# Optimization experiments

Measured on AMD Instinct MI355X. Metric: run time of the kernel, lower is better.

The kernel has to match this reference:

```python
import jax, jax.numpy as jnp
import numpy as np

D_MODEL, N_HEADS, D_HEAD = 512, 8, 64
NUM_BITS, C_TABLES, PHI_SCALE, MAX_EXP, EPS = 8, 2, 0.1, 4, 1e-6
B, T = 2, 1024


def setup_inputs() -> dict:
    key = jax.random.key(0)
    ks = jax.random.split(key, 7)
    x = jax.random.normal(ks[0], (B, T, D_MODEL), dtype=jnp.float32)
    w_std = 0.02
    Wq = jax.random.normal(ks[1], (D_MODEL, D_MODEL), dtype=jnp.float32) * w_std
    Wk = jax.random.normal(ks[2], (D_MODEL, D_MODEL), dtype=jnp.float32) * w_std
    Wv = jax.random.normal(ks[3], (D_MODEL, D_MODEL), dtype=jnp.float32) * w_std
    Wo = jax.random.normal(ks[4], (D_MODEL, D_MODEL), dtype=jnp.float32) * w_std
    bo = jnp.zeros((D_MODEL,), dtype=jnp.float32)
    # 'positive' init: strictly positive lookup values so phi acts as a kernel feature map
    phi_table = jax.random.uniform(ks[5], (C_TABLES, 2 ** NUM_BITS), dtype=jnp.float32) * 0.5 + 0.01
    return {"x": x, "Wq": Wq, "Wk": Wk, "Wv": Wv, "Wo": Wo, "bo": bo, "phi_table": phi_table}


def _ternary_weight(W):
    # quantize to {-1,0,1} * power-of-two scale (exponent clipped to +/- MAX_EXP), STE-style
    alpha = jnp.mean(jnp.abs(W)) + 1e-12
    e = jnp.clip(jnp.round(jnp.log2(alpha)), -MAX_EXP, MAX_EXP)
    s = jnp.exp2(e)
    Wt = jnp.clip(jnp.round(W / s), -1.0, 1.0) * s
    return W + jax.lax.stop_gradient(Wt - W)


def _ternary_linear(x, W, b=None):
    y = jnp.einsum('btd,ed->bte', x, _ternary_weight(W))
    return y if b is None else y + b


def _phi(x, table):
    # structured lookup activation: sum of c sub-tables indexed at dyadically scaled quantizations
    L = table.shape[1]
    off = L // 2
    y = jnp.zeros_like(x)
    for j in range(table.shape[0]):
        idx = jnp.clip(jnp.round(x / (PHI_SCALE * (2.0 ** j))).astype(jnp.int32) + off, 0, L - 1)
        y = y + table[j][idx]
    return x + jax.lax.stop_gradient(y - x)  # STE: forward = lookup, backward = identity


def reference(x, Wq, Wk, Wv, Wo, bo, phi_table):
    Bsz, Tn, _ = x.shape
    Q = _ternary_linear(x, Wq)
    K = _ternary_linear(x, Wk)
    V = _ternary_linear(x, Wv)

    def split_heads(t):
        return t.reshape(Bsz, Tn, N_HEADS, D_HEAD).transpose(0, 2, 1, 3)  # (B,H,T,d)

    Q, K, V = split_heads(Q), split_heads(K), split_heads(V)
    phiQ = _phi(Q, phi_table)
    phiK = _phi(K, phi_table)

    # causal linear attention via cumulative outer products (faithful to original)
    kv = jnp.einsum('bhnd,bhne->bhnde', phiK, V)            # (B,H,T,d,d)
    kv_cum = jnp.cumsum(kv, axis=2)
    out = jnp.einsum('bhnd,bhnde->bhne', phiQ, kv_cum)       # (B,H,T,d)
    k_cum = jnp.cumsum(phiK, axis=2)
    Z = jnp.clip(jnp.sum(phiQ * k_cum, axis=-1, keepdims=True), EPS, None)
    out = out / Z

    out = out.transpose(0, 2, 1, 3).reshape(Bsz, Tn, D_MODEL)
    return _ternary_linear(out, Wo, bo)
```

## Files before the change

### kernel.cpp

```cpp
#include <hip/hip_runtime.h>
#include <stdint.h>

typedef __bf16 bf16;
typedef __bf16 v8bf __attribute__((ext_vector_type(8)));
typedef float v4f __attribute__((ext_vector_type(4)));

#define T_SEQ   1024
#define D_MODEL 512
#define N_HEADS 8
#define D_HEAD  64
#define B_SZ    2
#define BH      (B_SZ * N_HEADS)
#define CHUNK   128
#define NCHUNK  (T_SEQ / CHUNK)
#define WN      (D_MODEL * D_MODEL)

__device__ __forceinline__ void lds16(const void* g, void* l) {
    __builtin_amdgcn_global_load_lds(
        (const __attribute__((address_space(1))) uint32_t*)g,
        (__attribute__((address_space(3))) uint32_t*)l, 16, 0, 0);
}

struct PreArgs { const float* w[4]; float* partial; const float* x; bf16* xb; };

__global__ __launch_bounds__(256) void k_pre(PreArgs a) {
    const int bid = blockIdx.x, tid = threadIdx.x;
    if (bid < 256) {
        const int mid = bid >> 6, blk = bid & 63;
        const float* __restrict__ W = a.w[mid];
        float sabs = 0.f;
        #pragma unroll
        for (int k = 0; k < 4; ++k) {
            float4 v = ((const float4*)W)[blk * 1024 + k * 256 + tid];
            sabs += fabsf(v.x) + fabsf(v.y) + fabsf(v.z) + fabsf(v.w);
        }
        __shared__ float red[256];
        red[tid] = sabs;
        __syncthreads();
        for (int s = 128; s > 0; s >>= 1) {
            if (tid < s) red[tid] += red[tid + s];
            __syncthreads();
        }
        if (tid == 0) a.partial[mid * 64 + blk] = red[0];
    } else {
        const int i = (bid - 256) * 256 + tid;
        float4 v = ((const float4*)a.x)[i];
        union { uint2 u; bf16 h[4]; } H;
        H.h[0] = (bf16)v.x; H.h[1] = (bf16)v.y;
        H.h[2] = (bf16)v.z; H.h[3] = (bf16)v.w;
        ((uint2*)a.xb)[i] = H.u;
    }
}

struct WqArgs { const float* w[4]; bf16* wt[4]; const float* partial; };

__global__ __launch_bounds__(256) void k_wquant(WqArgs a) {
    const int mid = blockIdx.y, blk = blockIdx.x, tid = threadIdx.x;
    const float* __restrict__ W = a.w[mid];
    bf16* __restrict__ Wt = a.wt[mid];
    __shared__ float sv;
    if (tid < 64) {
        float p = a.partial[mid * 64 + tid];
        #pragma unroll
        for (int w = 1; w < 64; w <<= 1) p += __shfl_xor(p, w);
        if (tid == 0) {
            float alpha = p / (float)WN + 1e-12f;
            float e = rintf(log2f(alpha));
            e = fminf(4.f, fmaxf(-4.f, e));
            sv = exp2f(e);
        }
    }
    __syncthreads();
    const float s = sv;
    const float inv_s = 1.f / s;
    #pragma unroll
    for (int k = 0; k < 4; ++k) {
        const int idx = blk * 1024 + k * 256 + tid;
        float4 v = ((const float4*)W)[idx];
        float vv[4] = {v.x, v.y, v.z, v.w};
        union { uint2 u; bf16 h[4]; } o;
        #pragma unroll
        for (int j = 0; j < 4; ++j) {
            float r = rintf(vv[j] * inv_s);
            r = fminf(1.f, fmaxf(-1.f, r));
            o.h[j] = (bf16)(r * s);
        }
        ((uint2*)Wt)[idx] = o.u;
    }
}

__device__ __forceinline__ void gemm64(
        const char* __restrict__ Ab, const char* __restrict__ Bb,
        bf16* As, bf16* Bs, v4f acc[4]) {
    const int tid = threadIdx.x;
    const int wm = tid >> 6, lane = tid & 63;
    const int q = lane >> 4, r = lane & 15;
    const int lrow = lane >> 3;
    const int schunk = (lane & 7) ^ lrow;
    const int r7 = r & 7;

    for (int k0 = 0; k0 < 512; k0 += 64) {
        #pragma unroll
        for (int j = 0; j < 2; ++j) {
            const int seg = wm * 2 + j;
            const int row = seg * 8 + lrow;
            const size_t goff = (size_t)row * 1024 + (size_t)k0 * 2 + schunk * 16;
            lds16(Ab + goff, (char*)As + (seg << 10));
            lds16(Bb + goff, (char*)Bs + (seg << 10));
        }
        __syncthreads();
        #pragma unroll
        for (int s = 0; s < 2; ++s) {
            const int co = ((s * 4 + q) ^ r7) * 8;
            v8bf ah = *(const v8bf*)&As[(wm * 16 + r) * 64 + co];
            v8bf bb[4];
            #pragma unroll
            for (int v = 0; v < 4; ++v)
                bb[v] = *(const v8bf*)&Bs[(v * 16 + r) * 64 + co];
            #pragma unroll
            for (int v = 0; v < 4; ++v)
                acc[v] = __builtin_amdgcn_mfma_f32_16x16x32_bf16(ah, bb[v], acc[v], 0, 0, 0);
        }
        __syncthreads();
    }
}

struct Qkv2Args {
    const bf16* xb; const bf16* wstk;
    const float* table;
    bf16* phiqB; bf16* phikB; bf16* phikT; bf16* vbufT;
};

__global__ __launch_bounds__(256) void k_qkv2(Qkv2Args a) {
    __shared__ bf16 As[64 * 64] __attribute__((aligned(16)));
    __shared__ bf16 Bs[64 * 64] __attribute__((aligned(16)));
    __shared__ float tab[512];
    const int tid = threadIdx.x;
    const int tm = blockIdx.x, tn = blockIdx.y;
    const int z = tn >> 3;
    if (z < 2) { tab[tid] = a.table[tid]; tab[tid + 256] = a.table[tid + 256]; }

    v4f acc[4];
    #pragma unroll
    for (int v = 0; v < 4; ++v) acc[v] = (v4f){0.f, 0.f, 0.f, 0.f};

    gemm64((const char*)(a.xb + (size_t)(tm * 64) * 512),
           (const char*)(a.wstk + (size_t)(tn * 64) * 512), As, Bs, acc);

    const int wm = tid >> 6, lane = tid & 63;
    const int q = lane >> 4, r = lane & 15;
    const int h = tn & 7;
    const int mb = tm * 64;
    const int b = mb >> 10, tpos0 = mb & 1023;
    const int bh = b * 8 + h;
    const int tpos = tpos0 + wm * 16 + q * 4;

    if (z < 2) {
        #pragma unroll
        for (int v = 0; v < 4; ++v) {
            const int d = v * 16 + r;
            union { uint2 pu; bf16 h4[4]; } P;
            #pragma unroll
            for (int i = 0; i < 4; ++i) {
                float val = acc[v][i];
                int i0 = (int)rintf(val / 0.1f) + 128;
                i0 = min(255, max(0, i0));
                int i1 = (int)rintf(val / 0.2f) + 128;
                i1 = min(255, max(0, i1));
                val = tab[i0] + tab[256 + i1];
                As[(wm * 16 + q * 4 + i) * 64 + d] = (bf16)val;
                P.h4[i] = (bf16)val;
            }
            if (z == 1)
                *(uint2*)&a.phikT[((size_t)bh * 64 + d) * 1024 + tpos] = P.pu;
        }
        __syncthreads();
        bf16* dst = (z == 0) ? a.phiqB : a.phikB;
        #pragma unroll
        for (int k = 0; k < 2; ++k) {
            const int idx = k * 256 + tid;
            const int row = idx >> 3, cb = (idx & 7) * 8;
            *(uint4*)&dst[((size_t)bh * 1024 + tpos0 + row) * 64 + cb] =
                *(const uint4*)&As[row * 64 + cb];
        }
    } else {
        #pragma unroll
        for (int v = 0; v < 4; ++v) {
            const int d = v * 16 + r;
            union { uint2 pu; bf16 h4[4]; } P;
            #pragma unroll
            for (int i = 0; i < 4; ++i) P.h4[i] = (bf16)acc[v][i];
            *(uint2*)&a.vbufT[((size_t)bh * 64 + d) * 1024 + tpos] = P.pu;
        }
    }
}

__global__ __launch_bounds__(256) void k_attn(
        const bf16* __restrict__ phiqB, const bf16* __restrict__ phikB,
        const bf16* __restrict__ phikT, const bf16* __restrict__ vbufT,
        bf16* __restrict__ attn) {
    const int ntile = blockIdx.x, c = blockIdx.y, bh = blockIdx.z;
    __shared__ char smem[56064] __attribute__((aligned(16)));
    bf16* pqs  = (bf16*)smem;
    bf16* kv0s = (bf16*)(smem + 9216);
    bf16* Pbs  = (bf16*)smem;
    bf16* pks  = (bf16*)(smem + 18432);
    bf16* vts  = (bf16*)(smem + 36864);
    bf16* tB   = (bf16*)(smem + 18432);
    bf16* tA   = (bf16*)(smem + 36864);
    float* kc0s = (float*)(smem + 54272);
    float* Zrow = (float*)(smem + 54528);
    float* Zp   = (float*)(smem + 54784);
    float* Zs   = (float*)(smem + 55808);

    const int tid = threadIdx.x;
    const int wid = tid >> 6, lane = tid & 63;
    const int q = lane >> 4, r = lane & 15;
    const size_t tbase = (size_t)bh * 1024 + c * 128;
    const int t0 = ntile * 64;

    #pragma unroll
    for (int k = 0; k < 2; ++k) {
        const int idx = k * 256 + tid;
        const int row = idx >> 3, col = (idx & 7) * 8;
        *(uint4*)&pqs[row * 72 + col] =
            *(const uint4*)&phiqB[(tbase + t0 + row) * 64 + col];
    }

    v4f kvacc[4];
    #pragma unroll
    for (int v = 0; v < 4; ++v) kvacc[v] = (v4f){0.f, 0.f, 0.f, 0.f};
    float kcp = 0.f;
    const int srow = tid >> 2, scol = (tid & 3) * 32;
    const int kd = tid & 63, ktq = tid >> 6;
    for (int cc = 0; cc < c; ++cc) {
        __syncthreads();
        #pragma unroll
        for (int j = 0; j < 4; ++j) {
            *(uint4*)&tB[srow * 136 + scol + j * 8] =
                *(const uint4*)&phikT[((size_t)bh * 64 + srow) * 1024 + cc * 128 + scol + j * 8];
            *(uint4*)&tA[srow * 136 + scol + j * 8] =
                *(const uint4*)&vbufT[((size_t)bh * 64 + srow) * 1024 + cc * 128 + scol + j * 8];
        }
        __syncthreads();
        #pragma unroll
        for (int kk = 0; kk < 4; ++kk) {
            v8bf av = *(const v8bf*)&tA[(wid * 16 + r) * 136 + kk * 32 + q * 8];
            #pragma unroll
            for (int v = 0; v < 4; ++v) {
                v8bf bd = *(const v8bf*)&tB[(v * 16 + r) * 136 + kk * 32 + q * 8];
                kvacc[v] = __builtin_amdgcn_mfma_f32_16x16x32_bf16(av, bd, kvacc[v], 0, 0, 0);
            }
        }
        #pragma unroll
        for (int j4 = 0; j4 < 4; ++j4) {
            v8bf p = *(const v8bf*)&tB[kd * 136 + ktq * 32 + j4 * 8];
            #pragma unroll
            for (int jj = 0; jj < 8; ++jj) kcp += (float)p[jj];
        }
    }
    #pragma unroll
    for (int v = 0; v < 4; ++v)
        #pragma unroll
        for (int i = 0; i < 4; ++i)
            kv0s[(wid * 16 + q * 4 + i) * 72 + v * 16 + r] = (bf16)kvacc[v][i];
    Zp[ktq * 64 + kd] = kcp;
    __syncthreads();

    #pragma unroll
    for (int k = 0; k < 4; ++k) {
        const int idx = k * 256 + tid;
        const int row = idx >> 3, col = (idx & 7) * 8;
        *(uint4*)&pks[row * 72 + col] =
            *(const uint4*)&phikB[(tbase + row) * 64 + col];
        const int row2 = idx >> 4, col2 = (idx & 15) * 8;
        *(uint4*)&vts[row2 * 136 + col2] =
            *(const uint4*)&vbufT[((size_t)bh * 64 + row2) * 1024 + c * 128 + col2];
    }
    if (tid < 64)
        kc0s[tid] = Zp[tid] + Zp[64 + tid] + Zp[128 + tid] + Zp[192 + tid];
    __syncthreads();

    v4f oacc[4], sacc[8];
    #pragma unroll
    for (int t = 0; t < 4; ++t) oacc[t] = (v4f){0.f, 0.f, 0.f, 0.f};
    #pragma unroll
    for (int u = 0; u < 8; ++u) sacc[u] = (v4f){0.f, 0.f, 0.f, 0.f};
    const int nmt = (ntile == 0) ? 4 : 8;

    #pragma unroll
    for (int kk = 0; kk < 2; ++kk) {
        v8bf af = *(const v8bf*)&pqs[(wid * 16 + r) * 72 + kk * 32 + q * 8];
        #pragma unroll
        for (int t = 0; t < 4; ++t) {
            v8bf bfr = *(const v8bf*)&kv0s[(t * 16 + r) * 72 + kk * 32 + q * 8];
            oacc[t] = __builtin_amdgcn_mfma_f32_16x16x32_bf16(af, bfr, oacc[t], 0, 0, 0);
        }
        #pragma unroll
        for (int u = 0; u < 8; ++u) {
            if (u < nmt) {
                v8bf bk = *(const v8bf*)&pks[(u * 16 + r) * 72 + kk * 32 + q * 8];
                sacc[u] = __builtin_amdgcn_mfma_f32_16x16x32_bf16(af, bk, sacc[u], 0, 0, 0);
            }
        }
    }
    {
        float z0 = 0.f;
        #pragma unroll
        for (int j = 0; j < 16; ++j)
            z0 += (float)pqs[lane * 72 + wid * 16 + j] * kc0s[wid * 16 + j];
        Zp[wid * 64 + lane] = z0;
    }
    __syncthreads();

    float zi[4] = {0.f, 0.f, 0.f, 0.f};
    #pragma unroll
    for (int u = 0; u < 8; ++u) {
        if (u < nmt) {
            const int m = u * 16 + r;
            #pragma unroll
            for (int i = 0; i < 4; ++i) {
                const int nloc = t0 + wid * 16 + q * 4 + i;
                const float sv = (m <= nloc) ? sacc[u][i] : 0.f;
                zi[i] += sv;
                Pbs[(wid * 16 + q * 4 + i) * 136 + m] = (bf16)sv;
            }
        }
    }
    #pragma unroll
    for (int w = 1; w < 16; w <<= 1) {
        #pragma unroll
        for (int i = 0; i < 4; ++i) zi[i] += __shfl_xor(zi[i], w);
    }
    if (r == 0) {
        #pragma unroll
        for (int i = 0; i < 4; ++i) Zrow[wid * 16 + q * 4 + i] = zi[i];
    }
    __syncthreads();

    if (tid < 64)
        Zs[tid] = fmaxf(Zrow[tid] + Zp[tid] + Zp[64 + tid] + Zp[128 + tid] + Zp[192 + tid],
                        1e-6f);
    __syncthreads();

    const int nkk = (ntile == 0) ? 2 : 4;
    #pragma unroll
    for (int kk = 0; kk < 4; ++kk) {
        if (kk < nkk) {
            v8bf af = *(const v8bf*)&Pbs[(wid * 16 + r) * 136 + kk * 32 + q * 8];
            #pragma unroll
            for (int t = 0; t < 4; ++t) {
                v8bf bfr = *(const v8bf*)&vts[(t * 16 + r) * 136 + kk * 32 + q * 8];
                oacc[t] = __builtin_amdgcn_mfma_f32_16x16x32_bf16(af, bfr, oacc[t], 0, 0, 0);
            }
        }
    }

    const int b = bh >> 3, h = bh & 7;
    #pragma unroll
    for (int t = 0; t < 4; ++t) {
        const int e = t * 16 + r;
        #pragma unroll
        for (int i = 0; i < 4; ++i) {
            const int row = wid * 16 + q * 4 + i;
            const float val = oacc[t][i] / Zs[row];
            const size_t mtok = (size_t)b * 1024 + c * 128 + t0 + row;
            attn[mtok * 512 + h * 64 + e] = (bf16)val;
        }
    }
}

struct OArgs { const bf16* attn; const bf16* wo; const float* bo; float* y; };

__global__ __launch_bounds__(256) void k_oproj(OArgs a) {
    __shared__ bf16 As[64 * 64] __attribute__((aligned(16)));
    __shared__ bf16 Bs[64 * 64] __attribute__((aligned(16)));
    v4f acc[4];
    #pragma unroll
    for (int v = 0; v < 4; ++v) acc[v] = (v4f){0.f, 0.f, 0.f, 0.f};
    gemm64((const char*)(a.attn + (size_t)(blockIdx.x * 64) * 512),
           (const char*)(a.wo + (size_t)(blockIdx.y * 64) * 512), As, Bs, acc);

    const int tid = threadIdx.x;
    const int wm = tid >> 6, lane = tid & 63;
    const int q = lane >> 4, r = lane & 15;
    #pragma unroll
    for (int v = 0; v < 4; ++v) {
        const int n = blockIdx.y * 64 + v * 16 + r;
        const float bias = a.bo[n];
        #pragma unroll
        for (int i = 0; i < 4; ++i) {
            const int m = blockIdx.x * 64 + wm * 16 + q * 4 + i;
            a.y[(size_t)m * 512 + n] = acc[v][i] + bias;
        }
    }
}

extern "C" void kernel_launch(void* const* d_in, const int* in_sizes, int n_in,
                              void* d_out, int out_size, void* d_ws, size_t ws_size,
                              hipStream_t stream) {
    const float* x   = (const float*)d_in[0];
    const float* Wq  = (const float*)d_in[1];
    const float* Wk  = (const float*)d_in[2];
    const float* Wv  = (const float*)d_in[3];
    const float* Wo  = (const float*)d_in[4];
    const float* bo  = (const float*)d_in[5];
    const float* tab = (const float*)d_in[6];

    uint8_t* w = (uint8_t*)d_ws;
    bf16* wt     = (bf16*)w;
    bf16* xb     = wt + 4 * WN;
    bf16* phiqB  = xb + 1048576;
    bf16* phikB  = phiqB + (size_t)16 * 1024 * 64;
    bf16* phikT  = phikB + (size_t)16 * 1024 * 64;
    bf16* vbufT  = phikT + (size_t)16 * 64 * 1024;
    bf16* attn   = vbufT + (size_t)16 * 64 * 1024;
    float* partial = (float*)(attn + (size_t)2048 * 512);

    PreArgs pr;
    pr.w[0] = Wq; pr.w[1] = Wk; pr.w[2] = Wv; pr.w[3] = Wo;
    pr.partial = partial; pr.x = x; pr.xb = xb;
    k_pre<<<dim3(1280), dim3(256), 0, stream>>>(pr);

    WqArgs qa;
    qa.w[0] = Wq; qa.w[1] = Wk; qa.w[2] = Wv; qa.w[3] = Wo;
    qa.wt[0] = wt; qa.wt[1] = wt + WN; qa.wt[2] = wt + 2 * WN; qa.wt[3] = wt + 3 * WN;
    qa.partial = partial;
    k_wquant<<<dim3(64, 4), dim3(256), 0, stream>>>(qa);

    Qkv2Args pa{ xb, wt, tab, phiqB, phikB, phikT, vbufT };
    k_qkv2<<<dim3(32, 24), dim3(256), 0, stream>>>(pa);

    k_attn<<<dim3(2, NCHUNK, BH), dim3(256), 0, stream>>>(phiqB, phikB, phikT, vbufT, attn);

    OArgs oa{ attn, wt + 3 * WN, bo, (float*)d_out };
    k_oproj<<<dim3(32, 8), dim3(256), 0, stream>>>(oa);
}
```

Before: 106.4 us.

## Fuse weight ternarization and x bf16 cast into GEMM tile loads

Removes the separate weight-quantization kernel and the x-to-bf16 conversion. The QKV and output-projection GEMMs now load fp32 x and raw weights directly, quantize and convert them in registers, and store swizzled bf16 tiles to LDS. Each block recomputes the power-of-two scale from the per-block partial sums. This saves two launches and the bf16 workspace round trip, but doubles global bytes per tile load and replaces async global-to-LDS loads with register-staged stores plus redundant per-block quantization ALU work.

```diff
diff --git a/kernel.cpp b/kernel.cpp
--- a/kernel.cpp
+++ b/kernel.cpp
@@ -21,83 +21,96 @@
         (__attribute__((address_space(3))) uint32_t*)l, 16, 0, 0);
 }
 
-struct PreArgs { const float* w[4]; float* partial; const float* x; bf16* xb; };
-
-__global__ __launch_bounds__(256) void k_pre(PreArgs a) {
+struct AlphaArgs { const float* w[4]; float* partial; };
+
+__global__ __launch_bounds__(256) void k_alpha(AlphaArgs a) {
     const int bid = blockIdx.x, tid = threadIdx.x;
-    if (bid < 256) {
-        const int mid = bid >> 6, blk = bid & 63;
-        const float* __restrict__ W = a.w[mid];
-        float sabs = 0.f;
-        #pragma unroll
-        for (int k = 0; k < 4; ++k) {
-            float4 v = ((const float4*)W)[blk * 1024 + k * 256 + tid];
-            sabs += fabsf(v.x) + fabsf(v.y) + fabsf(v.z) + fabsf(v.w);
-        }
-        __shared__ float red[256];
-        red[tid] = sabs;
-        __syncthreads();
-        for (int s = 128; s > 0; s >>= 1) {
-            if (tid < s) red[tid] += red[tid + s];
-            __syncthreads();
-        }
-        if (tid == 0) a.partial[mid * 64 + blk] = red[0];
-    } else {
-        const int i = (bid - 256) * 256 + tid;
-        float4 v = ((const float4*)a.x)[i];
-        union { uint2 u; bf16 h[4]; } H;
-        H.h[0] = (bf16)v.x; H.h[1] = (bf16)v.y;
-        H.h[2] = (bf16)v.z; H.h[3] = (bf16)v.w;
-        ((uint2*)a.xb)[i] = H.u;
-    }
-}
-
-struct WqArgs { const float* w[4]; bf16* wt[4]; const float* partial; };
-
-__global__ __launch_bounds__(256) void k_wquant(WqArgs a) {
-    const int mid = blockIdx.y, blk = blockIdx.x, tid = threadIdx.x;
+    const int mid = bid >> 6, blk = bid & 63;
     const float* __restrict__ W = a.w[mid];
-    bf16* __restrict__ Wt = a.wt[mid];
-    __shared__ float sv;
-    if (tid < 64) {
-        float p = a.partial[mid * 64 + tid];
-        #pragma unroll
-        for (int w = 1; w < 64; w <<= 1) p += __shfl_xor(p, w);
-        if (tid == 0) {
-            float alpha = p / (float)WN + 1e-12f;
-            float e = rintf(log2f(alpha));
-            e = fminf(4.f, fmaxf(-4.f, e));
-            sv = exp2f(e);
-        }
-    }
-    __syncthreads();
-    const float s = sv;
-    const float inv_s = 1.f / s;
+    float sabs = 0.f;
     #pragma unroll
     for (int k = 0; k < 4; ++k) {
-        const int idx = blk * 1024 + k * 256 + tid;
-        float4 v = ((const float4*)W)[idx];
-        float vv[4] = {v.x, v.y, v.z, v.w};
-        union { uint2 u; bf16 h[4]; } o;
-        #pragma unroll
-        for (int j = 0; j < 4; ++j) {
-            float r = rintf(vv[j] * inv_s);
-            r = fminf(1.f, fmaxf(-1.f, r));
-            o.h[j] = (bf16)(r * s);
-        }
-        ((uint2*)Wt)[idx] = o.u;
-    }
-}
-
-__device__ __forceinline__ void gemm64(
-        const char* __restrict__ Ab, const char* __restrict__ Bb,
-        bf16* As, bf16* Bs, v4f acc[4]) {
+        float4 v = ((const float4*)W)[blk * 1024 + k * 256 + tid];
+        sabs += fabsf(v.x) + fabsf(v.y) + fabsf(v.z) + fabsf(v.w);
+    }
+    __shared__ float red[256];
+    red[tid] = sabs;
+    __syncthreads();
+    for (int s = 128; s > 0; s >>= 1) {
+        if (tid < s) red[tid] += red[tid + s];
+        __syncthreads();
+    }
+    if (tid == 0) a.partial[mid * 64 + blk] = red[0];
+}
+
+__device__ __forceinline__ float alpha_scale(const float* partial, int mid) {
+    const int lane = threadIdx.x & 63;
+    float p = partial[mid * 64 + lane];
+    #pragma unroll
+    for (int w = 1; w < 64; w <<= 1) p += __shfl_xor(p, w);
+    float alpha = p / (float)WN + 1e-12f;
+    float e = fminf(4.f, fmaxf(-4.f, rintf(log2f(alpha))));
+    return exp2f(e);
+}
+
+__device__ __forceinline__ void gemm64_f32(
+        const float* __restrict__ Abase, const float* __restrict__ Bbase,
+        float s, float inv_s, bf16* As, bf16* Bs, v4f acc[4]) {
+    const int tid = threadIdx.x;
+    const int wm = tid >> 6, lane = tid & 63;
+    const int q = lane >> 4, r = lane & 15;
+    const int r7 = r & 7;
+    const int srow = tid >> 2;
+
+    for (int k0 = 0; k0 < 512; k0 += 64) {
+        #pragma unroll
+        for (int cp = 0; cp < 2; ++cp) {
+            const int lc = (tid & 3) + cp * 4;
+            const float* sa = Abase + srow * 512 + k0 + lc * 8;
+            const float* sb = Bbase + srow * 512 + k0 + lc * 8;
+            float4 a0 = *(const float4*)sa, a1 = *(const float4*)(sa + 4);
+            float4 b0 = *(const float4*)sb, b1 = *(const float4*)(sb + 4);
+            union { uint4 u; bf16 h[8]; } PA, PB;
+            float av[8] = {a0.x, a0.y, a0.z, a0.w, a1.x, a1.y, a1.z, a1.w};
+            float bv[8] = {b0.x, b0.y, b0.z, b0.w, b1.x, b1.y, b1.z, b1.w};
+            #pragma unroll
+            for (int j = 0; j < 8; ++j) {
+                PA.h[j] = (bf16)av[j];
+                float rr = rintf(bv[j] * inv_s);
+                rr = fminf(1.f, fmaxf(-1.f, rr));
+                PB.h[j] = (bf16)(rr * s);
+            }
+            const int pc = lc ^ (srow & 7);
+            *(uint4*)((char*)As + srow * 128 + pc * 16) = PA.u;
+            *(uint4*)((char*)Bs + srow * 128 + pc * 16) = PB.u;
+        }
+        __syncthreads();
+        #pragma unroll
+        for (int ss = 0; ss < 2; ++ss) {
+            const int co = ((ss * 4 + q) ^ r7) * 8;
+            v8bf ah = *(const v8bf*)&As[(wm * 16 + r) * 64 + co];
+            v8bf bb[4];
+            #pragma unroll
+            for (int v = 0; v < 4; ++v)
+                bb[v] = *(const v8bf*)&Bs[(v * 16 + r) * 64 + co];
+            #pragma unroll
+            for (int v = 0; v < 4; ++v)
+                acc[v] = __builtin_amdgcn_mfma_f32_16x16x32_bf16(ah, bb[v], acc[v], 0, 0, 0);
+        }
+        __syncthreads();
+    }
+}
+
+__device__ __forceinline__ void gemm64_bf16A(
+        const char* __restrict__ Ab, const float* __restrict__ Bbase,
+        float s, float inv_s, bf16* As, bf16* Bs, v4f acc[4]) {
     const int tid = threadIdx.x;
     const int wm = tid >> 6, lane = tid & 63;
     const int q = lane >> 4, r = lane & 15;
     const int lrow = lane >> 3;
     const int schunk = (lane & 7) ^ lrow;
     const int r7 = r & 7;
+    const int srow = tid >> 2;
 
     for (int k0 = 0; k0 < 512; k0 += 64) {
         #pragma unroll
@@ -106,12 +119,27 @@
             const int row = seg * 8 + lrow;
             const size_t goff = (size_t)row * 1024 + (size_t)k0 * 2 + schunk * 16;
             lds16(Ab + goff, (char*)As + (seg << 10));
-            lds16(Bb + goff, (char*)Bs + (seg << 10));
-        }
-        __syncthreads();
-        #pragma unroll
-        for (int s = 0; s < 2; ++s) {
-            const int co = ((s * 4 + q) ^ r7) * 8;
+        }
+        #pragma unroll
+        for (int cp = 0; cp < 2; ++cp) {
+            const int lc = (tid & 3) + cp * 4;
+            const float* sb = Bbase + srow * 512 + k0 + lc * 8;
+            float4 b0 = *(const float4*)sb, b1 = *(const float4*)(sb + 4);
+            union { uint4 u; bf16 h[8]; } PB;
+            float bv[8] = {b0.x, b0.y, b0.z, b0.w, b1.x, b1.y, b1.z, b1.w};
+            #pragma unroll
+            for (int j = 0; j < 8; ++j) {
+                float rr = rintf(bv[j] * inv_s);
+                rr = fminf(1.f, fmaxf(-1.f, rr));
+                PB.h[j] = (bf16)(rr * s);
+            }
+            const int pc = lc ^ (srow & 7);
+            *(uint4*)((char*)Bs + srow * 128 + pc * 16) = PB.u;
+        }
+        __syncthreads();
+        #pragma unroll
+        for (int ss = 0; ss < 2; ++ss) {
+            const int co = ((ss * 4 + q) ^ r7) * 8;
             v8bf ah = *(const v8bf*)&As[(wm * 16 + r) * 64 + co];
             v8bf bb[4];
             #pragma unroll
@@ -125,13 +153,13 @@
     }
 }
 
-struct Qkv2Args {
-    const bf16* xb; const bf16* wstk;
+struct QkvArgs {
+    const float* x; const float* w[3]; const float* partial;
     const float* table;
     bf16* phiqB; bf16* phikB; bf16* phikT; bf16* vbufT;
 };
 
-__global__ __launch_bounds__(256) void k_qkv2(Qkv2Args a) {
+__global__ __launch_bounds__(256) void k_qkv(QkvArgs a) {
     __shared__ bf16 As[64 * 64] __attribute__((aligned(16)));
     __shared__ bf16 Bs[64 * 64] __attribute__((aligned(16)));
     __shared__ float tab[512];
@@ -140,12 +168,16 @@
     const int z = tn >> 3;
     if (z < 2) { tab[tid] = a.table[tid]; tab[tid + 256] = a.table[tid + 256]; }
 
+    const float s = alpha_scale(a.partial, z);
+    const float inv_s = 1.f / s;
+
     v4f acc[4];
     #pragma unroll
     for (int v = 0; v < 4; ++v) acc[v] = (v4f){0.f, 0.f, 0.f, 0.f};
 
-    gemm64((const char*)(a.xb + (size_t)(tm * 64) * 512),
-           (const char*)(a.wstk + (size_t)(tn * 64) * 512), As, Bs, acc);
+    gemm64_f32(a.x + (size_t)(tm * 64) * 512,
+               a.w[z] + (size_t)((tn & 7) * 64) * 512,
+               s, inv_s, As, Bs, acc);
 
     const int wm = tid >> 6, lane = tid & 63;
     const int q = lane >> 4, r = lane & 15;
@@ -370,16 +402,20 @@
     }
 }
 
-struct OArgs { const bf16* attn; const bf16* wo; const float* bo; float* y; };
+struct OArgs { const bf16* attn; const float* wo; const float* partial;
+               const float* bo; float* y; };
 
 __global__ __launch_bounds__(256) void k_oproj(OArgs a) {
     __shared__ bf16 As[64 * 64] __attribute__((aligned(16)));
     __shared__ bf16 Bs[64 * 64] __attribute__((aligned(16)));
+    const float s = alpha_scale(a.partial, 3);
+    const float inv_s = 1.f / s;
     v4f acc[4];
     #pragma unroll
     for (int v = 0; v < 4; ++v) acc[v] = (v4f){0.f, 0.f, 0.f, 0.f};
-    gemm64((const char*)(a.attn + (size_t)(blockIdx.x * 64) * 512),
-           (const char*)(a.wo + (size_t)(blockIdx.y * 64) * 512), As, Bs, acc);
+    gemm64_bf16A((const char*)(a.attn + (size_t)(blockIdx.x * 64) * 512),
+                 a.wo + (size_t)(blockIdx.y * 64) * 512,
+                 s, inv_s, As, Bs, acc);
 
     const int tid = threadIdx.x;
     const int wm = tid >> 6, lane = tid & 63;
@@ -408,31 +444,26 @@
     const float* tab = (const float*)d_in[6];
 
     uint8_t* w = (uint8_t*)d_ws;
-    bf16* wt     = (bf16*)w;
-    bf16* xb     = wt + 4 * WN;
-    bf16* phiqB  = xb + 1048576;
+    bf16* phiqB  = (bf16*)w;
     bf16* phikB  = phiqB + (size_t)16 * 1024 * 64;
     bf16* phikT  = phikB + (size_t)16 * 1024 * 64;
     bf16* vbufT  = phikT + (size_t)16 * 64 * 1024;
     bf16* attn   = vbufT + (size_t)16 * 64 * 1024;
     float* partial = (float*)(attn + (size_t)2048 * 512);
 
-    PreArgs pr;
-    pr.w[0] = Wq; pr.w[1] = Wk; pr.w[2] = Wv; pr.w[3] = Wo;
-    pr.partial = partial; pr.x = x; pr.xb = xb;
-    k_pre<<<dim3(1280), dim3(256), 0, stream>>>(pr);
-
-    WqArgs qa;
-    qa.w[0] = Wq; qa.w[1] = Wk; qa.w[2] = Wv; qa.w[3] = Wo;
-    qa.wt[0] = wt; qa.wt[1] = wt + WN; qa.wt[2] = wt + 2 * WN; qa.wt[3] = wt + 3 * WN;
-    qa.partial = partial;
-    k_wquant<<<dim3(64, 4), dim3(256), 0, stream>>>(qa);
-
-    Qkv2Args pa{ xb, wt, tab, phiqB, phikB, phikT, vbufT };
-    k_qkv2<<<dim3(32, 24), dim3(256), 0, stream>>>(pa);
+    AlphaArgs aa;
+    aa.w[0] = Wq; aa.w[1] = Wk; aa.w[2] = Wv; aa.w[3] = Wo;
+    aa.partial = partial;
+    k_alpha<<<dim3(256), dim3(256), 0, stream>>>(aa);
+
+    QkvArgs pa;
+    pa.x = x; pa.w[0] = Wq; pa.w[1] = Wk; pa.w[2] = Wv;
+    pa.partial = partial; pa.table = tab;
+    pa.phiqB = phiqB; pa.phikB = phikB; pa.phikT = phikT; pa.vbufT = vbufT;
+    k_qkv<<<dim3(32, 24), dim3(256), 0, stream>>>(pa);
 
     k_attn<<<dim3(2, NCHUNK, BH), dim3(256), 0, stream>>>(phiqB, phikB, phikT, vbufT, attn);
 
-    OArgs oa{ attn, wt + 3 * WN, bo, (float*)d_out };
+    OArgs oa{ attn, Wo, partial, bo, (float*)d_out };
     k_oproj<<<dim3(32, 8), dim3(256), 0, stream>>>(oa);
 }
```

Result: slower. 110.9 us (+4.3%).

## Precompute per-chunk KV outer products in separate kernel, prefix-sum in attention

Applied to the files above, without the earlier changes.

Adds a k_chunkmm kernel that computes each chunk's phiK^T·V product and phiK column sums once, stored in fp32. k_attn then builds its inter-chunk state by summing the stored per-chunk results for all earlier chunks instead of recomputing every earlier chunk's MFMA products. This removes quadratic redundant matmul work, since the old code recomputed earlier chunks for every later chunk and for both n-tiles. The cost is an extra kernel launch and fp32 workspace traffic for the per-chunk state.

```diff
diff --git a/kernel.cpp b/kernel.cpp
--- a/kernel.cpp
+++ b/kernel.cpp
@@ -195,10 +195,66 @@
     }
 }
 
+__global__ __launch_bounds__(256) void k_chunkmm(
+        const bf16* __restrict__ phikT, const bf16* __restrict__ vbufT,
+        float* __restrict__ kvT, float* __restrict__ ksc) {
+    const int c = blockIdx.x, bh = blockIdx.y;
+    __shared__ bf16 tB[64 * 136] __attribute__((aligned(16)));
+    __shared__ bf16 tA[64 * 136] __attribute__((aligned(16)));
+    __shared__ float kcr[256];
+    const int tid = threadIdx.x;
+    const int wid = tid >> 6, lane = tid & 63;
+    const int q = lane >> 4, r = lane & 15;
+    const int srow = tid >> 2, scol = (tid & 3) * 32;
+
+    #pragma unroll
+    for (int j = 0; j < 4; ++j) {
+        *(uint4*)&tB[srow * 136 + scol + j * 8] =
+            *(const uint4*)&phikT[((size_t)bh * 64 + srow) * 1024 + c * 128 + scol + j * 8];
+        *(uint4*)&tA[srow * 136 + scol + j * 8] =
+            *(const uint4*)&vbufT[((size_t)bh * 64 + srow) * 1024 + c * 128 + scol + j * 8];
+    }
+    __syncthreads();
+
+    v4f kvacc[4];
+    #pragma unroll
+    for (int v = 0; v < 4; ++v) kvacc[v] = (v4f){0.f, 0.f, 0.f, 0.f};
+    #pragma unroll
+    for (int kk = 0; kk < 4; ++kk) {
+        v8bf av = *(const v8bf*)&tA[(wid * 16 + r) * 136 + kk * 32 + q * 8];
+        #pragma unroll
+        for (int v = 0; v < 4; ++v) {
+            v8bf bd = *(const v8bf*)&tB[(v * 16 + r) * 136 + kk * 32 + q * 8];
+            kvacc[v] = __builtin_amdgcn_mfma_f32_16x16x32_bf16(av, bd, kvacc[v], 0, 0, 0);
+        }
+    }
+    {
+        float kcp = 0.f;
+        const int kd = tid & 63, ktq = tid >> 6;
+        #pragma unroll
+        for (int j4 = 0; j4 < 4; ++j4) {
+            v8bf p = *(const v8bf*)&tB[kd * 136 + ktq * 32 + j4 * 8];
+            #pragma unroll
+            for (int jj = 0; jj < 8; ++jj) kcp += (float)p[jj];
+        }
+        kcr[ktq * 64 + kd] = kcp;
+    }
+    __syncthreads();
+    const size_t ob = ((size_t)bh * 8 + c) * 4096;
+    #pragma unroll
+    for (int v = 0; v < 4; ++v)
+        #pragma unroll
+        for (int i = 0; i < 4; ++i)
+            kvT[ob + (size_t)(wid * 16 + q * 4 + i) * 64 + v * 16 + r] = kvacc[v][i];
+    if (tid < 64)
+        ksc[((size_t)bh * 8 + c) * 64 + tid] =
+            kcr[tid] + kcr[64 + tid] + kcr[128 + tid] + kcr[192 + tid];
+}
+
 __global__ __launch_bounds__(256) void k_attn(
         const bf16* __restrict__ phiqB, const bf16* __restrict__ phikB,
-        const bf16* __restrict__ phikT, const bf16* __restrict__ vbufT,
-        bf16* __restrict__ attn) {
+        const bf16* __restrict__ vbufT, const float* __restrict__ kvT,
+        const float* __restrict__ ksc, bf16* __restrict__ attn) {
     const int ntile = blockIdx.x, c = blockIdx.y, bh = blockIdx.z;
     __shared__ char smem[56064] __attribute__((aligned(16)));
     bf16* pqs  = (bf16*)smem;
@@ -206,8 +262,6 @@
     bf16* Pbs  = (bf16*)smem;
     bf16* pks  = (bf16*)(smem + 18432);
     bf16* vts  = (bf16*)(smem + 36864);
-    bf16* tB   = (bf16*)(smem + 18432);
-    bf16* tA   = (bf16*)(smem + 36864);
     float* kc0s = (float*)(smem + 54272);
     float* Zrow = (float*)(smem + 54528);
     float* Zp   = (float*)(smem + 54784);
@@ -226,47 +280,29 @@
         *(uint4*)&pqs[row * 72 + col] =
             *(const uint4*)&phiqB[(tbase + t0 + row) * 64 + col];
     }
-
-    v4f kvacc[4];
-    #pragma unroll
-    for (int v = 0; v < 4; ++v) kvacc[v] = (v4f){0.f, 0.f, 0.f, 0.f};
-    float kcp = 0.f;
-    const int srow = tid >> 2, scol = (tid & 3) * 32;
-    const int kd = tid & 63, ktq = tid >> 6;
-    for (int cc = 0; cc < c; ++cc) {
-        __syncthreads();
-        #pragma unroll
-        for (int j = 0; j < 4; ++j) {
-            *(uint4*)&tB[srow * 136 + scol + j * 8] =
-                *(const uint4*)&phikT[((size_t)bh * 64 + srow) * 1024 + cc * 128 + scol + j * 8];
-            *(uint4*)&tA[srow * 136 + scol + j * 8] =
-                *(const uint4*)&vbufT[((size_t)bh * 64 + srow) * 1024 + cc * 128 + scol + j * 8];
-        }
-        __syncthreads();
-        #pragma unroll
-        for (int kk = 0; kk < 4; ++kk) {
-            v8bf av = *(const v8bf*)&tA[(wid * 16 + r) * 136 + kk * 32 + q * 8];
-            #pragma unroll
-            for (int v = 0; v < 4; ++v) {
-                v8bf bd = *(const v8bf*)&tB[(v * 16 + r) * 136 + kk * 32 + q * 8];
-                kvacc[v] = __builtin_amdgcn_mfma_f32_16x16x32_bf16(av, bd, kvacc[v], 0, 0, 0);
+    {
+        const int e = tid >> 2, db = (tid & 3) * 16;
+        float accp[16];
+        #pragma unroll
+        for (int j = 0; j < 16; ++j) accp[j] = 0.f;
+        for (int cc = 0; cc < c; ++cc) {
+            const float* src = kvT + ((size_t)bh * 8 + cc) * 4096 + e * 64 + db;
+            #pragma unroll
+            for (int k4 = 0; k4 < 4; ++k4) {
+                float4 f = *(const float4*)(src + 4 * k4);
+                accp[4 * k4]     += f.x; accp[4 * k4 + 1] += f.y;
+                accp[4 * k4 + 2] += f.z; accp[4 * k4 + 3] += f.w;
             }
         }
-        #pragma unroll
-        for (int j4 = 0; j4 < 4; ++j4) {
-            v8bf p = *(const v8bf*)&tB[kd * 136 + ktq * 32 + j4 * 8];
-            #pragma unroll
-            for (int jj = 0; jj < 8; ++jj) kcp += (float)p[jj];
-        }
-    }
-    #pragma unroll
-    for (int v = 0; v < 4; ++v)
-        #pragma unroll
-        for (int i = 0; i < 4; ++i)
-            kv0s[(wid * 16 + q * 4 + i) * 72 + v * 16 + r] = (bf16)kvacc[v][i];
-    Zp[ktq * 64 + kd] = kcp;
-    __syncthreads();
-
+        union { uint4 u; bf16 h8[8]; } U0, U1;
+        #pragma unroll
+        for (int j = 0; j < 8; ++j) {
+            U0.h8[j] = (bf16)accp[j];
+            U1.h8[j] = (bf16)accp[8 + j];
+        }
+        *(uint4*)&kv0s[e * 72 + db] = U0.u;
+        *(uint4*)&kv0s[e * 72 + db + 8] = U1.u;
+    }
     #pragma unroll
     for (int k = 0; k < 4; ++k) {
         const int idx = k * 256 + tid;
@@ -277,8 +313,11 @@
         *(uint4*)&vts[row2 * 136 + col2] =
             *(const uint4*)&vbufT[((size_t)bh * 64 + row2) * 1024 + c * 128 + col2];
     }
-    if (tid < 64)
-        kc0s[tid] = Zp[tid] + Zp[64 + tid] + Zp[128 + tid] + Zp[192 + tid];
+    if (tid < 64) {
+        float s = 0.f;
+        for (int cc = 0; cc < c; ++cc) s += ksc[((size_t)bh * 8 + cc) * 64 + tid];
+        kc0s[tid] = s;
+    }
     __syncthreads();
 
     v4f oacc[4], sacc[8];
@@ -415,7 +454,9 @@
     bf16* phikT  = phikB + (size_t)16 * 1024 * 64;
     bf16* vbufT  = phikT + (size_t)16 * 64 * 1024;
     bf16* attn   = vbufT + (size_t)16 * 64 * 1024;
-    float* partial = (float*)(attn + (size_t)2048 * 512);
+    float* kvT   = (float*)(attn + (size_t)2048 * 512);
+    float* ksc   = kvT + (size_t)16 * 8 * 4096;
+    float* partial = ksc + 16 * 8 * 64;
 
     PreArgs pr;
     pr.w[0] = Wq; pr.w[1] = Wk; pr.w[2] = Wv; pr.w[3] = Wo;
@@ -431,7 +472,8 @@
     Qkv2Args pa{ xb, wt, tab, phiqB, phikB, phikT, vbufT };
     k_qkv2<<<dim3(32, 24), dim3(256), 0, stream>>>(pa);
 
-    k_attn<<<dim3(2, NCHUNK, BH), dim3(256), 0, stream>>>(phiqB, phikB, phikT, vbufT, attn);
+    k_chunkmm<<<dim3(NCHUNK, BH), dim3(256), 0, stream>>>(phikT, vbufT, kvT, ksc);
+    k_attn<<<dim3(2, NCHUNK, BH), dim3(256), 0, stream>>>(phiqB, phikB, vbufT, kvT, ksc, attn);
 
     OArgs oa{ attn, wt + 3 * WN, bo, (float*)d_out };
     k_oproj<<<dim3(32, 8), dim3(256), 0, stream>>>(oa);
```

Result: faster. 103.4 us (-2.8%).
